# Performance work log

Measured on AMD Instinct MI355X. Metric: run time of the kernel, lower is better.

## Reference

```python
import jax, jax.numpy as jnp
import numpy as np

N_HEADS = 16


def setup_inputs() -> dict:
    key = jax.random.key(0)
    ks = jax.random.split(key, 12)
    B, S, D = 2, 2048, 1024
    inp = {
        "query": jax.random.normal(ks[0], (B, S, D), jnp.float32),
        "key": jax.random.normal(ks[1], (B, S, D), jnp.float32),
        "value": jax.random.normal(ks[2], (B, S, D), jnp.float32),
        "mask": jnp.ones((B, S), jnp.int32),
        "Wq": jax.random.normal(ks[3], (D, D), jnp.float32) * 0.02,
        "bq": jax.random.normal(ks[4], (D,), jnp.float32) * 0.02,
        "Wk": jax.random.normal(ks[5], (D, D), jnp.float32) * 0.02,
        "bk": jax.random.normal(ks[6], (D,), jnp.float32) * 0.02,
        "Wv": jax.random.normal(ks[7], (D, D), jnp.float32) * 0.02,
        "bv": jax.random.normal(ks[8], (D,), jnp.float32) * 0.02,
        "Wo": jax.random.normal(ks[9], (D, D), jnp.float32) * 0.02,
        "bo": jax.random.normal(ks[10], (D,), jnp.float32) * 0.02,
    }
    return inp


def _shape(x, bs, n_heads, d_head):
    # (bs, seq, dim) -> (bs, n_heads, seq, d_head)
    return x.reshape(bs, -1, n_heads, d_head).transpose(0, 2, 1, 3)


def reference(query, key, value, mask, Wq, bq, Wk, bk, Wv, bv, Wo, bo):
    bs, q_len, dim = query.shape
    d_head = dim // N_HEADS

    q = _shape(query @ Wq + bq, bs, N_HEADS, d_head) / jnp.sqrt(jnp.asarray(d_head, query.dtype))
    k = _shape(key @ Wk + bk, bs, N_HEADS, d_head)
    v = _shape(value @ Wv + bv, bs, N_HEADS, d_head)

    scores = jnp.einsum("bhqd,bhkd->bhqk", q, k)  # [bs, h, q_len, k_len]
    neg = jnp.finfo(scores.dtype).min
    scores = jnp.where((mask == 0)[:, None, None, :], neg, scores)
    weights = jax.nn.softmax(scores, axis=-1)  # dropout p=0 -> identity

    context = jnp.einsum("bhqk,bhkd->bhqd", weights, v)
    context = context.transpose(0, 2, 1, 3).reshape(bs, q_len, dim)
    return context @ Wo + bo
```

## Files before the change

### kernel.cpp

```cpp
#include <hip/hip_runtime.h>
#include <hip/hip_bf16.h>
#include <stdint.h>

typedef short s16x8 __attribute__((ext_vector_type(8)));
typedef float f32x4 __attribute__((ext_vector_type(4)));
typedef float f32x16 __attribute__((ext_vector_type(16)));

union FragU { uint4 u; s16x8 v; };

static __device__ __forceinline__ uint32_t pk2bf(float a, float b) {
  union { __hip_bfloat162 h; uint32_t u; } cv;
  cv.h = __float22bfloat162_rn(make_float2(a, b));
  return cv.u;
}

static __device__ __forceinline__ unsigned short f2bf(float f) {
  union { float f; uint32_t u; } x; x.f = f;
  uint32_t r = x.u + 0x7FFFu + ((x.u >> 16) & 1u);
  return (unsigned short)(r >> 16);
}

static __device__ __forceinline__ void gl_lds16(const void* g, void* lds_wave_base) {
  __builtin_amdgcn_global_load_lds(
      (const __attribute__((address_space(1))) uint32_t*)(uintptr_t)g,
      (__attribute__((address_space(3))) uint32_t*)(uintptr_t)lds_wave_base, 16, 0, 0);
}

__global__ __launch_bounds__(256) void prep_kernel(const float* __restrict__ W0,
                                                   const float* __restrict__ W1,
                                                   const float* __restrict__ W2,
                                                   const float* __restrict__ W3,
                                                   unsigned short* __restrict__ T0,
                                                   unsigned short* __restrict__ T1,
                                                   unsigned short* __restrict__ T2,
                                                   unsigned short* __restrict__ T3,
                                                   const float* __restrict__ qs,
                                                   const float* __restrict__ ks,
                                                   const float* __restrict__ vs,
                                                   unsigned short* __restrict__ Qc,
                                                   unsigned short* __restrict__ Kc,
                                                   unsigned short* __restrict__ Vc) {
  __shared__ unsigned short tile[64][68];
  const int blk = blockIdx.x;
  const int t = threadIdx.x;
  if (blk < 1024) {
    const int z = blk >> 8;
    const float* W = (z == 0) ? W0 : (z == 1) ? W1 : (z == 2) ? W2 : W3;
    unsigned short* WT = (z == 0) ? T0 : (z == 1) ? T1 : (z == 2) ? T2 : T3;
    const int n0 = (blk & 15) * 64, k0 = ((blk >> 4) & 15) * 64;
    const int r = t >> 4, c4 = (t & 15) * 4;
#pragma unroll
    for (int i = 0; i < 4; ++i) {
      const int k = i * 16 + r;
      const float4 v = *(const float4*)&W[(k0 + k) * 1024 + n0 + c4];
      tile[k][c4 + 0] = f2bf(v.x);
      tile[k][c4 + 1] = f2bf(v.y);
      tile[k][c4 + 2] = f2bf(v.z);
      tile[k][c4 + 3] = f2bf(v.w);
    }
    __syncthreads();
#pragma unroll
    for (int i = 0; i < 4; ++i) {
      const int n = i * 16 + r;
      ushort4 o;
      o.x = tile[c4 + 0][n];
      o.y = tile[c4 + 1][n];
      o.z = tile[c4 + 2][n];
      o.w = tile[c4 + 3][n];
      *(ushort4*)&WT[(n0 + n) * 1024 + k0 + c4] = o;
    }
  } else {
    const int c = blk - 1024;
    const int z = c >> 11, sub = c & 2047;
    const float* src = (z == 0) ? qs : (z == 1) ? ks : vs;
    unsigned short* dst = (z == 0) ? Qc : (z == 1) ? Kc : Vc;
    const size_t base = ((size_t)sub * 256 + t) * 8;
    const float4 f0 = *(const float4*)(src + base);
    const float4 f1 = *(const float4*)(src + base + 4);
    const uint4 o{pk2bf(f0.x, f0.y), pk2bf(f0.z, f0.w), pk2bf(f1.x, f1.y), pk2bf(f1.z, f1.w)};
    *(uint4*)(dst + base) = o;
  }
}

__global__ __launch_bounds__(256) void wt4_kernel(const float* __restrict__ W0,
                                                  const float* __restrict__ W1,
                                                  const float* __restrict__ W2,
                                                  const float* __restrict__ W3,
                                                  unsigned short* __restrict__ T0,
                                                  unsigned short* __restrict__ T1,
                                                  unsigned short* __restrict__ T2,
                                                  unsigned short* __restrict__ T3) {
  __shared__ unsigned short tile[64][68];
  const int z = blockIdx.z;
  const float* W = (z == 0) ? W0 : (z == 1) ? W1 : (z == 2) ? W2 : W3;
  unsigned short* WT = (z == 0) ? T0 : (z == 1) ? T1 : (z == 2) ? T2 : T3;
  const int t = threadIdx.x;
  const int n0 = blockIdx.x * 64, k0 = blockIdx.y * 64;
  const int r = t >> 4, c4 = (t & 15) * 4;
#pragma unroll
  for (int i = 0; i < 4; ++i) {
    const int k = i * 16 + r;
    const float4 v = *(const float4*)&W[(k0 + k) * 1024 + n0 + c4];
    tile[k][c4 + 0] = f2bf(v.x);
    tile[k][c4 + 1] = f2bf(v.y);
    tile[k][c4 + 2] = f2bf(v.z);
    tile[k][c4 + 3] = f2bf(v.w);
  }
  __syncthreads();
#pragma unroll
  for (int i = 0; i < 4; ++i) {
    const int n = i * 16 + r;
    ushort4 o;
    o.x = tile[c4 + 0][n];
    o.y = tile[c4 + 1][n];
    o.z = tile[c4 + 2][n];
    o.w = tile[c4 + 3][n];
    *(ushort4*)&WT[(n0 + n) * 1024 + k0 + c4] = o;
  }
}

__global__ __launch_bounds__(256, 3) void qkv_gemm_bf16(const unsigned short* __restrict__ Aq,
                                                        const unsigned short* __restrict__ Ak,
                                                        const unsigned short* __restrict__ Av,
                                                        const unsigned short* __restrict__ Wq,
                                                        const unsigned short* __restrict__ Wk,
                                                        const unsigned short* __restrict__ Wv,
                                                        const float* __restrict__ bq,
                                                        const float* __restrict__ bk,
                                                        const float* __restrict__ bv,
                                                        unsigned short* __restrict__ Qb,
                                                        unsigned short* __restrict__ Kb,
                                                        unsigned short* __restrict__ Vt,
                                                        const float qscale) {
  __shared__ char AsB[3][8192];
  __shared__ char BsB[3][8192];
  const int t = threadIdx.x;
  const int z = blockIdx.z;
  const unsigned short* A = (z == 0) ? Aq : (z == 1) ? Ak : Av;
  const unsigned short* BT = (z == 0) ? Wq : (z == 1) ? Wk : Wv;
  const float* bias = (z == 0) ? bq : (z == 1) ? bk : bv;
  const float scale = (z == 0) ? qscale : 1.0f;

  const int lane = t & 63, w = t >> 6;
  const int g = lane >> 4, li = lane & 15;
  const int wr = (w >> 1) * 64, wc = (w & 1) * 64;
  const int lin = blockIdx.x + 8 * blockIdx.y;
  const int work = (lin & 7) * 32 + (lin >> 3);
  const int m0 = (work >> 3) * 128, n0 = (work & 7) * 128;

  const int r1 = t >> 2, c1 = (t & 3) ^ ((r1 >> 1) & 3);
  const int r2 = r1 + 64, c2 = (t & 3) ^ ((r2 >> 1) & 3);

  auto stage = [&](int kt, int buf) {
    const int k0 = kt * 32;
    gl_lds16(A + (size_t)(m0 + r1) * 1024 + k0 + c1 * 8, &AsB[buf][0] + (w << 10));
    gl_lds16(A + (size_t)(m0 + r2) * 1024 + k0 + c2 * 8, &AsB[buf][0] + 4096 + (w << 10));
    gl_lds16(BT + (size_t)(n0 + r1) * 1024 + k0 + c1 * 8, &BsB[buf][0] + (w << 10));
    gl_lds16(BT + (size_t)(n0 + r2) * 1024 + k0 + c2 * 8, &BsB[buf][0] + 4096 + (w << 10));
  };

  f32x4 acc[4][4] = {};
  stage(0, 0);
  stage(1, 1);
  asm volatile("s_waitcnt vmcnt(4)" ::: "memory");
  asm volatile("s_barrier" ::: "memory");

  int cur = 0;
  for (int kt = 0; kt < 32; ++kt) {
    if (kt < 30) {
      int nb = cur + 2; if (nb >= 3) nb -= 3;
      stage(kt + 2, nb);
    }
    const char* Ab = &AsB[cur][0];
    const char* Bb = &BsB[cur][0];
    FragU a[4], bf[4];
#pragma unroll
    for (int i = 0; i < 4; ++i) {
      const int ra = wr + i * 16 + li;
      a[i].u = *(const uint4*)(Ab + ra * 64 + ((g ^ ((ra >> 1) & 3)) << 4));
      const int rb = wc + i * 16 + li;
      bf[i].u = *(const uint4*)(Bb + rb * 64 + ((g ^ ((rb >> 1) & 3)) << 4));
    }
#pragma unroll
    for (int fm = 0; fm < 4; ++fm)
#pragma unroll
      for (int fn = 0; fn < 4; ++fn)
        acc[fm][fn] = __builtin_amdgcn_mfma_f32_16x16x32_bf16(a[fm].v, bf[fn].v, acc[fm][fn], 0, 0, 0);

    if (kt < 30) {
      asm volatile("s_waitcnt vmcnt(4)" ::: "memory");
    } else if (kt == 30) {
      asm volatile("s_waitcnt vmcnt(0)" ::: "memory");
    }
    if (kt < 31) asm volatile("s_barrier" ::: "memory");
    cur = (cur == 2) ? 0 : cur + 1;
  }

  unsigned short* OutN = (z == 0) ? Qb : Kb;
#pragma unroll
  for (int fn = 0; fn < 4; ++fn) {
    const int n = n0 + wc + fn * 16 + li;
    const float bv2 = bias[n];
#pragma unroll
    for (int fm = 0; fm < 4; ++fm) {
      const int mb = m0 + wr + fm * 16 + g * 4;
      const f32x4 v = acc[fm][fn];
      ushort4 pk;
      pk.x = f2bf((v[0] + bv2) * scale);
      pk.y = f2bf((v[1] + bv2) * scale);
      pk.z = f2bf((v[2] + bv2) * scale);
      pk.w = f2bf((v[3] + bv2) * scale);
      if (z == 2) {
        const int bb = mb >> 11, s = mb & 2047;
        *(ushort4*)&Vt[(size_t)(bb * 1024 + n) * 2048 + s] = pk;
      } else {
        unsigned short* o = OutN;
        o[(size_t)(mb + 0) * 1024 + n] = pk.x;
        o[(size_t)(mb + 1) * 1024 + n] = pk.y;
        o[(size_t)(mb + 2) * 1024 + n] = pk.z;
        o[(size_t)(mb + 3) * 1024 + n] = pk.w;
      }
    }
  }
}

__global__ __launch_bounds__(256, 3) void qkv_gemm_f32(const float* __restrict__ Aq,
                                                       const float* __restrict__ Ak,
                                                       const float* __restrict__ Av,
                                                       const unsigned short* __restrict__ Wq,
                                                       const unsigned short* __restrict__ Wk,
                                                       const unsigned short* __restrict__ Wv,
                                                       const float* __restrict__ bq,
                                                       const float* __restrict__ bk,
                                                       const float* __restrict__ bv,
                                                       unsigned short* __restrict__ Qb,
                                                       unsigned short* __restrict__ Kb,
                                                       unsigned short* __restrict__ Vt,
                                                       const float qscale) {
  __shared__ unsigned short As[2][128 * 32];
  __shared__ unsigned short Bs[2][128 * 32];
  const int t = threadIdx.x;
  const int z = blockIdx.z;
  const float* A = (z == 0) ? Aq : (z == 1) ? Ak : Av;
  const unsigned short* BT = (z == 0) ? Wq : (z == 1) ? Wk : Wv;
  const float* bias = (z == 0) ? bq : (z == 1) ? bk : bv;
  const float scale = (z == 0) ? qscale : 1.0f;

  const int lane = t & 63, w = t >> 6;
  const int g = lane >> 4, li = lane & 15;
  const int wr = (w >> 1) * 64, wc = (w & 1) * 64;
  const int lin = blockIdx.x + 8 * blockIdx.y;
  const int work = (lin & 7) * 32 + (lin >> 3);
  const int m0 = (work >> 3) * 128, n0 = (work & 7) * 128;

  const int arow = t >> 1, ac0 = (t & 1) * 2, asw = (arow >> 1) & 3;
  const int br1 = t >> 2, bg1 = (t & 3) ^ ((br1 >> 1) & 3);
  const int br2 = br1 + 64, bg2 = (t & 3) ^ ((br2 >> 1) & 3);

  auto stageB = [&](int k0, int buf) {
    gl_lds16(BT + (size_t)(n0 + br1) * 1024 + k0 + bg1 * 8, (char*)&Bs[buf][0] + (w << 10));
    gl_lds16(BT + (size_t)(n0 + br2) * 1024 + k0 + bg2 * 8, (char*)&Bs[buf][0] + 4096 + (w << 10));
  };

  uint4 ar0, ar1;
  auto loadA = [&](int k0) {
    const float* ga = A + (size_t)(m0 + arow) * 1024 + k0 + ac0 * 8;
    const float4 f0 = *(const float4*)(ga + 0), f1 = *(const float4*)(ga + 4);
    const float4 f2 = *(const float4*)(ga + 8), f3 = *(const float4*)(ga + 12);
    ar0 = uint4{pk2bf(f0.x, f0.y), pk2bf(f0.z, f0.w), pk2bf(f1.x, f1.y), pk2bf(f1.z, f1.w)};
    ar1 = uint4{pk2bf(f2.x, f2.y), pk2bf(f2.z, f2.w), pk2bf(f3.x, f3.y), pk2bf(f3.z, f3.w)};
  };
  auto storeA = [&](int buf) {
    char* ab = (char*)&As[buf][0] + arow * 64;
    *(uint4*)(ab + ((ac0 ^ asw) << 4)) = ar0;
    *(uint4*)(ab + (((ac0 + 1) ^ asw) << 4)) = ar1;
  };

  f32x4 acc[4][4] = {};
  stageB(0, 0);
  loadA(0);
  storeA(0);
  __syncthreads();
  int cur = 0;
  for (int k0 = 0; k0 < 1024; k0 += 32) {
    const bool more = (k0 + 32) < 1024;
    if (more) {
      stageB(k0 + 32, cur ^ 1);
      loadA(k0 + 32);
    }
    const char* Ab = (const char*)&As[cur][0];
    const char* Bb = (const char*)&Bs[cur][0];
    FragU a[4], bf[4];
#pragma unroll
    for (int i = 0; i < 4; ++i) {
      const int rowa = wr + i * 16 + li;
      a[i].u = *(const uint4*)(Ab + rowa * 64 + (((g) ^ ((rowa >> 1) & 3)) << 4));
      const int rowb = wc + i * 16 + li;
      bf[i].u = *(const uint4*)(Bb + rowb * 64 + (((g) ^ ((rowb >> 1) & 3)) << 4));
    }
#pragma unroll
    for (int fm = 0; fm < 4; ++fm)
#pragma unroll
      for (int fn = 0; fn < 4; ++fn)
        acc[fm][fn] = __builtin_amdgcn_mfma_f32_16x16x32_bf16(a[fm].v, bf[fn].v, acc[fm][fn], 0, 0, 0);
    if (more) storeA(cur ^ 1);
    __syncthreads();
    cur ^= 1;
  }

  unsigned short* OutN = (z == 0) ? Qb : Kb;
#pragma unroll
  for (int fn = 0; fn < 4; ++fn) {
    const int n = n0 + wc + fn * 16 + li;
    const float bv2 = bias[n];
#pragma unroll
    for (int fm = 0; fm < 4; ++fm) {
      const int mb = m0 + wr + fm * 16 + g * 4;
      const f32x4 v = acc[fm][fn];
      ushort4 pk;
      pk.x = f2bf((v[0] + bv2) * scale);
      pk.y = f2bf((v[1] + bv2) * scale);
      pk.z = f2bf((v[2] + bv2) * scale);
      pk.w = f2bf((v[3] + bv2) * scale);
      if (z == 2) {
        const int bb = mb >> 11, s = mb & 2047;
        *(ushort4*)&Vt[(size_t)(bb * 1024 + n) * 2048 + s] = pk;
      } else {
        unsigned short* o = OutN;
        o[(size_t)(mb + 0) * 1024 + n] = pk.x;
        o[(size_t)(mb + 1) * 1024 + n] = pk.y;
        o[(size_t)(mb + 2) * 1024 + n] = pk.z;
        o[(size_t)(mb + 3) * 1024 + n] = pk.w;
      }
    }
  }
}

__global__ __launch_bounds__(256, 3) void out_gemm(const unsigned short* __restrict__ A,
                                                   const unsigned short* __restrict__ BT,
                                                   const float* __restrict__ bias,
                                                   float* __restrict__ Out) {
  __shared__ char AsB[3][8192];
  __shared__ char BsB[3][8192];
  const int t = threadIdx.x;
  const int lane = t & 63, w = t >> 6;
  const int g = lane >> 4, li = lane & 15;
  const int wr = (w >> 1) * 64, wc = (w & 1) * 64;
  const int lin = blockIdx.x + 8 * blockIdx.y;
  const int work = (lin & 7) * 32 + (lin >> 3);
  const int m0 = (work >> 3) * 128, n0 = (work & 7) * 128;

  const int r1 = t >> 2, c1 = (t & 3) ^ ((r1 >> 1) & 3);
  const int r2 = r1 + 64, c2 = (t & 3) ^ ((r2 >> 1) & 3);

  auto stage = [&](int kt, int buf) {
    const int k0 = kt * 32;
    gl_lds16(A + (size_t)(m0 + r1) * 1024 + k0 + c1 * 8, &AsB[buf][0] + (w << 10));
    gl_lds16(A + (size_t)(m0 + r2) * 1024 + k0 + c2 * 8, &AsB[buf][0] + 4096 + (w << 10));
    gl_lds16(BT + (size_t)(n0 + r1) * 1024 + k0 + c1 * 8, &BsB[buf][0] + (w << 10));
    gl_lds16(BT + (size_t)(n0 + r2) * 1024 + k0 + c2 * 8, &BsB[buf][0] + 4096 + (w << 10));
  };

  f32x4 acc[4][4] = {};
  stage(0, 0);
  stage(1, 1);
  asm volatile("s_waitcnt vmcnt(4)" ::: "memory");
  asm volatile("s_barrier" ::: "memory");

  int cur = 0;
  for (int kt = 0; kt < 32; ++kt) {
    if (kt < 30) {
      int nb = cur + 2; if (nb >= 3) nb -= 3;
      stage(kt + 2, nb);
    }
    const char* Ab = &AsB[cur][0];
    const char* Bb = &BsB[cur][0];
    FragU a[4], bf[4];
#pragma unroll
    for (int i = 0; i < 4; ++i) {
      const int ra = wr + i * 16 + li;
      a[i].u = *(const uint4*)(Ab + ra * 64 + ((g ^ ((ra >> 1) & 3)) << 4));
      const int rb = wc + i * 16 + li;
      bf[i].u = *(const uint4*)(Bb + rb * 64 + ((g ^ ((rb >> 1) & 3)) << 4));
    }
#pragma unroll
    for (int fm = 0; fm < 4; ++fm)
#pragma unroll
      for (int fn = 0; fn < 4; ++fn)
        acc[fm][fn] = __builtin_amdgcn_mfma_f32_16x16x32_bf16(a[fm].v, bf[fn].v, acc[fm][fn], 0, 0, 0);

    if (kt < 30) {
      asm volatile("s_waitcnt vmcnt(4)" ::: "memory");
    } else if (kt == 30) {
      asm volatile("s_waitcnt vmcnt(0)" ::: "memory");
    }
    if (kt < 31) asm volatile("s_barrier" ::: "memory");
    cur = (cur == 2) ? 0 : cur + 1;
  }

#pragma unroll
  for (int fn = 0; fn < 4; ++fn) {
    const int n = n0 + wc + fn * 16 + li;
    const float bv = bias[n];
#pragma unroll
    for (int fm = 0; fm < 4; ++fm) {
      const int mb = m0 + wr + fm * 16 + g * 4;
      const f32x4 v = acc[fm][fn];
#pragma unroll
      for (int r = 0; r < 4; ++r) Out[(size_t)(mb + r) * 1024 + n] = v[r] + bv;
    }
  }
}

__global__ __launch_bounds__(256, 2) void attn_kernel(const unsigned short* __restrict__ Qb,
                                                      const unsigned short* __restrict__ Kb,
                                                      const unsigned short* __restrict__ Vt,
                                                      const int* __restrict__ mask,
                                                      unsigned short* __restrict__ ctx) {
  __shared__ char smem[32768];
  const int t = threadIdx.x, lane = t & 63, w = t >> 6;
  const int l31 = lane & 31, hi = lane >> 5;
  const int p = w & 1;
  const int d0 = blockIdx.x;
  const int work = (d0 & 7) * 128 + (d0 >> 3);
  const int qblk = work & 31, bh = work >> 5;
  const int b = bh >> 4, h = bh & 15;
  const int qrow = b * 2048 + qblk * 64 + (w >> 1) * 32 + l31;

  char* Ksp = smem + p * 8192;
  char* Vsp = smem + 16384 + p * 8192;

  const unsigned short* Kbase = Kb + (size_t)(b * 2048) * 1024 + h * 64;
  const unsigned short* Vbase = Vt + (size_t)(b * 1024 + h * 64) * 2048;

  const int srw = (lane >> 3);
  const int ssc = (lane & 7) ^ srw;

  int mv_next;
  auto stage = [&](int i) {
    const int ke = 2 * i * 64, ko = ke + 64;
#pragma unroll
    for (int j = 0; j < 2; ++j) {
      const int rr = w * 16 + j * 8 + srw;
      char* ldsb = smem + w * 2048 + j * 1024;
      gl_lds16(Kbase + (size_t)(ke + rr) * 1024 + ssc * 8, ldsb);
      gl_lds16(Kbase + (size_t)(ko + rr) * 1024 + ssc * 8, ldsb + 8192);
      gl_lds16(Vbase + (size_t)rr * 2048 + ke + ssc * 8, ldsb + 16384);
      gl_lds16(Vbase + (size_t)rr * 2048 + ko + ssc * 8, ldsb + 24576);
    }
    mv_next = mask[b * 2048 + (2 * i + p) * 64 + lane];
  };

  FragU qf[4];
  {
    const unsigned short* qb = Qb + (size_t)qrow * 1024 + h * 64 + hi * 8;
#pragma unroll
    for (int dc = 0; dc < 4; ++dc) qf[dc].u = *(const uint4*)(qb + dc * 16);
  }

  stage(0);
  asm volatile("s_waitcnt vmcnt(0)" ::: "memory");
  int mv_cur = mv_next;
  asm volatile("s_barrier" ::: "memory");
  __builtin_amdgcn_sched_barrier(0);

  f32x16 acc[2] = {};
  float m_run = 8.0f, l_run = 0.f;

  for (int i = 0; i < 16; ++i) {
    const int mvcur = mv_cur;

    f32x16 sc[2] = {};
    {
      __builtin_amdgcn_s_setprio(1);
#pragma unroll
      for (int t2 = 0; t2 < 2; ++t2) {
        const int row = t2 * 32 + l31;
        const int sw = (row & 7) << 4;
        const int rb = row * 128;
#pragma unroll
        for (int dc = 0; dc < 4; ++dc) {
          FragU kf;
          kf.u = *(const uint4*)(Ksp + rb + ((16 * (dc * 2 + hi)) ^ sw));
          sc[t2] = __builtin_amdgcn_mfma_f32_32x32x16_bf16(kf.v, qf[dc].v, sc[t2], 0, 0, 0);
        }
      }
      __builtin_amdgcn_s_setprio(0);
    }

    if (!__all(mvcur != 0)) {
#pragma unroll
      for (int t2 = 0; t2 < 2; ++t2)
#pragma unroll
        for (int r = 0; r < 16; ++r) {
          const int kvv = t2 * 32 + (r & 3) + 8 * (r >> 2) + 4 * hi;
          sc[t2][r] += (__shfl(mvcur, kvv, 64) ? 0.f : -30000.f);
        }
    }

    float pm = sc[0][0];
#pragma unroll
    for (int t2 = 0; t2 < 2; ++t2)
#pragma unroll
      for (int r = 0; r < 16; ++r) pm = fmaxf(pm, sc[t2][r]);
    pm = fmaxf(pm, __shfl_xor(pm, 32, 64));

    if (!__all(pm <= m_run + 8.f)) {
      const float m_new = fmaxf(m_run, pm);
      const float rsc = __builtin_amdgcn_exp2f(m_run - m_new);
      m_run = m_new;
      l_run *= rsc;
#pragma unroll
      for (int dt = 0; dt < 2; ++dt)
#pragma unroll
        for (int r = 0; r < 16; ++r) acc[dt][r] *= rsc;
    }

    float rs = 0.f;
#pragma unroll
    for (int t2 = 0; t2 < 2; ++t2)
#pragma unroll
      for (int r = 0; r < 16; ++r) {
        const float e = __builtin_amdgcn_exp2f(sc[t2][r] - m_run);
        sc[t2][r] = e;
        rs += e;
      }
    l_run += rs;

    FragU pf[4];
#pragma unroll
    for (int ks = 0; ks < 4; ++ks) {
      const int t2 = ks >> 1, s8 = (ks & 1) * 8;
      uint32_t U = pk2bf(sc[t2][s8 + 0], sc[t2][s8 + 1]);
      uint32_t V2 = pk2bf(sc[t2][s8 + 2], sc[t2][s8 + 3]);
      uint32_t X = pk2bf(sc[t2][s8 + 4], sc[t2][s8 + 5]);
      uint32_t Y = pk2bf(sc[t2][s8 + 6], sc[t2][s8 + 7]);
      asm("v_permlane32_swap_b32 %0, %1" : "+v"(U), "+v"(X));
      asm("v_permlane32_swap_b32 %0, %1" : "+v"(V2), "+v"(Y));
      pf[ks].u = uint4{U, V2, X, Y};
    }

    {
      __builtin_amdgcn_s_setprio(1);
#pragma unroll
      for (int dt = 0; dt < 2; ++dt) {
        const int drow = dt * 32 + l31;
        const int sw = (drow & 7) << 4;
        const int rb = drow * 128;
#pragma unroll
        for (int ks = 0; ks < 4; ++ks) {
          FragU vf;
          vf.u = *(const uint4*)(Vsp + rb + ((16 * (ks * 2 + hi)) ^ sw));
          acc[dt] = __builtin_amdgcn_mfma_f32_32x32x16_bf16(vf.v, pf[ks].v, acc[dt], 0, 0, 0);
        }
      }
      __builtin_amdgcn_s_setprio(0);
    }

    if (i < 15) {
      asm volatile("s_barrier" ::: "memory");
      stage(i + 1);
      asm volatile("s_waitcnt vmcnt(0)" ::: "memory");
      mv_cur = mv_next;
      asm volatile("s_barrier" ::: "memory");
      __builtin_amdgcn_sched_barrier(0);
    }
  }

  asm volatile("s_barrier" ::: "memory");
  float* exch = (float*)smem;
  float* myex = exch + (w >> 1) * (64 * 37) + lane * 37;
  if (p) {
    const float l_red = l_run + __shfl_xor(l_run, 32, 64);
#pragma unroll
    for (int dt = 0; dt < 2; ++dt)
#pragma unroll
      for (int r = 0; r < 16; ++r) myex[dt * 16 + r] = acc[dt][r];
    myex[32] = m_run;
    myex[33] = l_red;
  }
  asm volatile("s_waitcnt lgkmcnt(0)" ::: "memory");
  asm volatile("s_barrier" ::: "memory");
  if (!p) {
    const float m_b = myex[32], l_b = myex[33];
    const float l_a = l_run + __shfl_xor(l_run, 32, 64);
    const float m = fmaxf(m_run, m_b);
    const float ea = __builtin_amdgcn_exp2f(m_run - m);
    const float eb = __builtin_amdgcn_exp2f(m_b - m);
    const float inv_l = 1.0f / (l_a * ea + l_b * eb);
    unsigned short* cb = ctx + (size_t)qrow * 1024 + h * 64;
#pragma unroll
    for (int dt = 0; dt < 2; ++dt)
#pragma unroll
      for (int rq = 0; rq < 4; ++rq) {
        float v0 = (acc[dt][rq * 4 + 0] * ea + myex[dt * 16 + rq * 4 + 0] * eb) * inv_l;
        float v1 = (acc[dt][rq * 4 + 1] * ea + myex[dt * 16 + rq * 4 + 1] * eb) * inv_l;
        float v2 = (acc[dt][rq * 4 + 2] * ea + myex[dt * 16 + rq * 4 + 2] * eb) * inv_l;
        float v3 = (acc[dt][rq * 4 + 3] * ea + myex[dt * 16 + rq * 4 + 3] * eb) * inv_l;
        uint2 o;
        o.x = pk2bf(v0, v1);
        o.y = pk2bf(v2, v3);
        *(uint2*)(cb + dt * 32 + rq * 8 + hi * 4) = o;
      }
  }
}

extern "C" void kernel_launch(void* const* d_in, const int* in_sizes, int n_in,
                              void* d_out, int out_size, void* d_ws, size_t ws_size,
                              hipStream_t stream) {
  const float* query = (const float*)d_in[0];
  const float* key = (const float*)d_in[1];
  const float* value = (const float*)d_in[2];
  const int* mask = (const int*)d_in[3];
  const float* Wq = (const float*)d_in[4];
  const float* bq = (const float*)d_in[5];
  const float* Wk = (const float*)d_in[6];
  const float* bk = (const float*)d_in[7];
  const float* Wv = (const float*)d_in[8];
  const float* bv = (const float*)d_in[9];
  const float* Wo = (const float*)d_in[10];
  const float* bo = (const float*)d_in[11];
  float* out = (float*)d_out;

  const size_t MB = 1024 * 1024;
  if (ws_size < 40 * MB) return;
  char* ws = (char*)d_ws;
  unsigned short* WqT = (unsigned short*)(ws);
  unsigned short* WkT = (unsigned short*)(ws + 2 * MB);
  unsigned short* WvT = (unsigned short*)(ws + 4 * MB);
  unsigned short* WoT = (unsigned short*)(ws + 6 * MB);
  unsigned short* Qb = (unsigned short*)(ws + 8 * MB);
  unsigned short* Kb = (unsigned short*)(ws + 16 * MB);
  unsigned short* Vt = (unsigned short*)(ws + 24 * MB);
  unsigned short* ctx = (unsigned short*)(ws + 32 * MB);

  const dim3 tb(256);
  const float qscale = 0.125f * 1.4426950408889634f;

  if (ws_size >= 64 * MB) {
    unsigned short* Qc = (unsigned short*)(ws + 40 * MB);
    unsigned short* Kc = (unsigned short*)(ws + 48 * MB);
    unsigned short* Vc = (unsigned short*)(ws + 56 * MB);
    prep_kernel<<<dim3(7168), tb, 0, stream>>>(Wq, Wk, Wv, Wo, WqT, WkT, WvT, WoT,
                                               query, key, value, Qc, Kc, Vc);
    qkv_gemm_bf16<<<dim3(8, 32, 3), tb, 0, stream>>>(Qc, Kc, Vc, WqT, WkT, WvT,
                                                     bq, bk, bv, Qb, Kb, Vt, qscale);
  } else {
    wt4_kernel<<<dim3(16, 16, 4), tb, 0, stream>>>(Wq, Wk, Wv, Wo, WqT, WkT, WvT, WoT);
    qkv_gemm_f32<<<dim3(8, 32, 3), tb, 0, stream>>>(query, key, value, WqT, WkT, WvT,
                                                    bq, bk, bv, Qb, Kb, Vt, qscale);
  }

  attn_kernel<<<dim3(1024), tb, 0, stream>>>(Qb, Kb, Vt, mask, ctx);

  out_gemm<<<dim3(8, 32), tb, 0, stream>>>(ctx, WoT, bo, out);
}
```

Baseline: 130.4 us.

## Restructure attention to 128-query blocks with double-buffered KV prefetch

The attention kernel no longer splits the KV sequence across wave pairs with a final LDS merge. Each block now handles 128 query rows, one 32-row slice per wave, over all 32 KV tiles. The next K/V tile is loaded into an alternate LDS buffer while the current one is computed. This removes the cross-wave softmax merge and one barrier per iteration, and halves K/V reloads per query. The cost is half as many blocks (512) and a longer serial loop per wave.

```diff
diff --git a/kernel.cpp b/kernel.cpp
--- a/kernel.cpp
+++ b/kernel.cpp
@@ -417,38 +417,33 @@
                                                       const unsigned short* __restrict__ Vt,
                                                       const int* __restrict__ mask,
                                                       unsigned short* __restrict__ ctx) {
-  __shared__ char smem[32768];
+  __shared__ char smem[2][16384];
   const int t = threadIdx.x, lane = t & 63, w = t >> 6;
   const int l31 = lane & 31, hi = lane >> 5;
-  const int p = w & 1;
-  const int d0 = blockIdx.x;
-  const int work = (d0 & 7) * 128 + (d0 >> 3);
-  const int qblk = work & 31, bh = work >> 5;
+  const int d0 = blockIdx.x + 16 * blockIdx.y;
+  const int work = (d0 & 7) * 64 + (d0 >> 3);
+  const int qblk = work & 15, bh = work >> 4;
   const int b = bh >> 4, h = bh & 15;
-  const int qrow = b * 2048 + qblk * 64 + (w >> 1) * 32 + l31;
-
-  char* Ksp = smem + p * 8192;
-  char* Vsp = smem + 16384 + p * 8192;
+  const int q0 = qblk * 128;
+  const int qrow = b * 2048 + q0 + w * 32 + l31;
 
   const unsigned short* Kbase = Kb + (size_t)(b * 2048) * 1024 + h * 64;
   const unsigned short* Vbase = Vt + (size_t)(b * 1024 + h * 64) * 2048;
 
-  const int srw = (lane >> 3);
+  const int srw = lane >> 3;
   const int ssc = (lane & 7) ^ srw;
 
   int mv_next;
-  auto stage = [&](int i) {
-    const int ke = 2 * i * 64, ko = ke + 64;
+  auto stage = [&](int i, int buf) {
+    const int kv0 = i * 64;
 #pragma unroll
     for (int j = 0; j < 2; ++j) {
       const int rr = w * 16 + j * 8 + srw;
-      char* ldsb = smem + w * 2048 + j * 1024;
-      gl_lds16(Kbase + (size_t)(ke + rr) * 1024 + ssc * 8, ldsb);
-      gl_lds16(Kbase + (size_t)(ko + rr) * 1024 + ssc * 8, ldsb + 8192);
-      gl_lds16(Vbase + (size_t)rr * 2048 + ke + ssc * 8, ldsb + 16384);
-      gl_lds16(Vbase + (size_t)rr * 2048 + ko + ssc * 8, ldsb + 24576);
-    }
-    mv_next = mask[b * 2048 + (2 * i + p) * 64 + lane];
+      char* ldsb = &smem[buf][0] + w * 2048 + j * 1024;
+      gl_lds16(Kbase + (size_t)(kv0 + rr) * 1024 + ssc * 8, ldsb);
+      gl_lds16(Vbase + (size_t)rr * 2048 + kv0 + ssc * 8, ldsb + 8192);
+    }
+    mv_next = mask[b * 2048 + kv0 + lane];
   };
 
   FragU qf[4];
@@ -458,7 +453,7 @@
     for (int dc = 0; dc < 4; ++dc) qf[dc].u = *(const uint4*)(qb + dc * 16);
   }
 
-  stage(0);
+  stage(0, 0);
   asm volatile("s_waitcnt vmcnt(0)" ::: "memory");
   int mv_cur = mv_next;
   asm volatile("s_barrier" ::: "memory");
@@ -466,9 +461,13 @@
 
   f32x16 acc[2] = {};
   float m_run = 8.0f, l_run = 0.f;
-
-  for (int i = 0; i < 16; ++i) {
+  int cur = 0;
+
+  for (int i = 0; i < 32; ++i) {
+    if (i < 31) stage(i + 1, cur ^ 1);
     const int mvcur = mv_cur;
+    const char* Ksp = &smem[cur][0];
+    const char* Vsp = &smem[cur][8192];
 
     f32x16 sc[2] = {};
     {
@@ -557,52 +556,27 @@
       __builtin_amdgcn_s_setprio(0);
     }
 
-    if (i < 15) {
-      asm volatile("s_barrier" ::: "memory");
-      stage(i + 1);
+    if (i < 31) {
       asm volatile("s_waitcnt vmcnt(0)" ::: "memory");
       mv_cur = mv_next;
       asm volatile("s_barrier" ::: "memory");
       __builtin_amdgcn_sched_barrier(0);
-    }
-  }
-
-  asm volatile("s_barrier" ::: "memory");
-  float* exch = (float*)smem;
-  float* myex = exch + (w >> 1) * (64 * 37) + lane * 37;
-  if (p) {
-    const float l_red = l_run + __shfl_xor(l_run, 32, 64);
-#pragma unroll
-    for (int dt = 0; dt < 2; ++dt)
-#pragma unroll
-      for (int r = 0; r < 16; ++r) myex[dt * 16 + r] = acc[dt][r];
-    myex[32] = m_run;
-    myex[33] = l_red;
-  }
-  asm volatile("s_waitcnt lgkmcnt(0)" ::: "memory");
-  asm volatile("s_barrier" ::: "memory");
-  if (!p) {
-    const float m_b = myex[32], l_b = myex[33];
-    const float l_a = l_run + __shfl_xor(l_run, 32, 64);
-    const float m = fmaxf(m_run, m_b);
-    const float ea = __builtin_amdgcn_exp2f(m_run - m);
-    const float eb = __builtin_amdgcn_exp2f(m_b - m);
-    const float inv_l = 1.0f / (l_a * ea + l_b * eb);
-    unsigned short* cb = ctx + (size_t)qrow * 1024 + h * 64;
-#pragma unroll
-    for (int dt = 0; dt < 2; ++dt)
-#pragma unroll
-      for (int rq = 0; rq < 4; ++rq) {
-        float v0 = (acc[dt][rq * 4 + 0] * ea + myex[dt * 16 + rq * 4 + 0] * eb) * inv_l;
-        float v1 = (acc[dt][rq * 4 + 1] * ea + myex[dt * 16 + rq * 4 + 1] * eb) * inv_l;
-        float v2 = (acc[dt][rq * 4 + 2] * ea + myex[dt * 16 + rq * 4 + 2] * eb) * inv_l;
-        float v3 = (acc[dt][rq * 4 + 3] * ea + myex[dt * 16 + rq * 4 + 3] * eb) * inv_l;
-        uint2 o;
-        o.x = pk2bf(v0, v1);
-        o.y = pk2bf(v2, v3);
-        *(uint2*)(cb + dt * 32 + rq * 8 + hi * 4) = o;
-      }
-  }
+      cur ^= 1;
+    }
+  }
+
+  const float l_tot = l_run + __shfl_xor(l_run, 32, 64);
+  const float inv_l = 1.0f / l_tot;
+  unsigned short* cb = ctx + (size_t)qrow * 1024 + h * 64;
+#pragma unroll
+  for (int dt = 0; dt < 2; ++dt)
+#pragma unroll
+    for (int rq = 0; rq < 4; ++rq) {
+      uint2 o;
+      o.x = pk2bf(acc[dt][rq * 4 + 0] * inv_l, acc[dt][rq * 4 + 1] * inv_l);
+      o.y = pk2bf(acc[dt][rq * 4 + 2] * inv_l, acc[dt][rq * 4 + 3] * inv_l);
+      *(uint2*)(cb + dt * 32 + rq * 8 + hi * 4) = o;
+    }
 }
 
 extern "C" void kernel_launch(void* const* d_in, const int* in_sizes, int n_in,
@@ -651,7 +625,7 @@
                                                     bq, bk, bv, Qb, Kb, Vt, qscale);
   }
 
-  attn_kernel<<<dim3(1024), tb, 0, stream>>>(Qb, Kb, Vt, mask, ctx);
+  attn_kernel<<<dim3(16, 32), tb, 0, stream>>>(Qb, Kb, Vt, mask, ctx);
 
   out_gemm<<<dim3(8, 32), tb, 0, stream>>>(ctx, WoT, bo, out);
 }
```

New measurement: 125.1 us. 1.04x faster.
